# Optimization experiments

Measured on AMD Instinct MI355X. Metric: run time of the kernel, lower is better.

Reference implementation:

```python
import jax, jax.numpy as jnp
import numpy as np

B, T, D, H, L, O = 512, 512, 128, 256, 2, 1


def setup_inputs() -> dict:
    key = jax.random.key(0)
    ks = jax.random.split(key, 10)
    s = lambda fan_in: 1.0 / np.sqrt(fan_in)
    return {
        "x": jax.random.normal(ks[0], (B, T, D), jnp.float32),
        "h0": jax.random.normal(ks[1], (L, B, H), jnp.float32),
        "c0": jax.random.normal(ks[2], (L, B, H), jnp.float32),
        "wi_0": jax.random.normal(ks[3], (D, 4 * H), jnp.float32) * s(D),
        "hi_0": jax.random.normal(ks[4], (H, 4 * H), jnp.float32) * s(H),
        "bias_0": jnp.zeros((4 * H,), jnp.float32),
        "wi_1": jax.random.normal(ks[5], (H, 4 * H), jnp.float32) * s(H),
        "hi_1": jax.random.normal(ks[6], (H, 4 * H), jnp.float32) * s(H),
        "bias_1": jnp.zeros((4 * H,), jnp.float32),
        "fc_w": jax.random.normal(ks[7], (H, O), jnp.float32) * s(H),
        "fc_b": jnp.zeros((O,), jnp.float32),
    }


def _lstm_cell(x_t, h, c, wi, hi, b):
    # x_t: [B, Din], h/c: [B, H]
    gates = x_t @ wi + h @ hi + b  # [B, 4H]
    i_t = jax.nn.sigmoid(gates[:, :H])
    f_t = jax.nn.sigmoid(gates[:, H:2 * H])
    g_t = jnp.tanh(gates[:, 2 * H:3 * H])
    o_t = jax.nn.sigmoid(gates[:, 3 * H:])
    c_new = f_t * c + i_t * g_t
    h_new = o_t * jnp.tanh(c_new)
    return h_new, c_new


def reference(x, h0, c0, wi_0, hi_0, bias_0, wi_1, hi_1, bias_1, fc_w, fc_b):
    xs = jnp.transpose(x, (1, 0, 2))  # [T, B, D]
    layers = ((wi_0, hi_0, bias_0), (wi_1, hi_1, bias_1))

    def step(carry, x_t):
        hs, cs = carry  # each [L, B, H]
        new_h, new_c = [], []
        inp = x_t
        for i, (wi, hi, b) in enumerate(layers):
            h, c = _lstm_cell(inp, hs[i], cs[i], wi, hi, b)
            new_h.append(h)
            new_c.append(c)
            inp = h
        return (jnp.stack(new_h), jnp.stack(new_c)), None

    (hs, _), _ = jax.lax.scan(step, (h0, c0), xs)
    return hs[-1] @ fc_w + fc_b  # [B, O]
```

## Files before the change

kernel.cpp:

```cpp
#include <hip/hip_runtime.h>


#define G4 1024

typedef __bf16 bf16x8 __attribute__((ext_vector_type(8)));
typedef float f32x4 __attribute__((ext_vector_type(4)));
typedef unsigned short u16x8 __attribute__((ext_vector_type(8)));

#define MFMA(a, b, c) __builtin_amdgcn_mfma_f32_16x16x32_bf16(a, b, c, 0, 0, 0)
#define GIDX(r, c) ((c) ^ ((((r) >> 2) & 1) << 4))

__device__ __forceinline__ unsigned short f2bf(float f) {
  unsigned u = __builtin_bit_cast(unsigned, f);
  u += 0x7fffu + ((u >> 16) & 1u);
  return (unsigned short)(u >> 16);
}
__device__ __forceinline__ float bf2f(unsigned v) {
  v <<= 16;
  return __builtin_bit_cast(float, v);
}
__device__ __forceinline__ float sigm(float x) { return 1.f / (1.f + __expf(-x)); }
__device__ __forceinline__ float tanh_(float x) {
  float e = __expf(-2.f * fabsf(x));
  float t = (1.f - e) / (1.f + e);
  return (x < 0.f) ? -t : t;
}

template <int IMM>
__device__ __forceinline__ unsigned g_load_i(const unsigned* p) {
  unsigned r;
  asm volatile("global_load_dword %0, %1, off offset:%c2 sc0 sc1"
               : "=v"(r) : "v"(p), "i"(IMM) : "memory");
  return r;
}
__device__ __forceinline__ void g_store1(unsigned* p, unsigned v) {
  asm volatile("global_store_dword %0, %1, off sc0 sc1" ::"v"(p), "v"(v) : "memory");
}
__device__ __forceinline__ unsigned long long g_load2(const unsigned* p) {
  unsigned long long r;
  asm volatile("global_load_dwordx2 %0, %1, off sc0 sc1"
               : "=v"(r) : "v"(p) : "memory");
  return r;
}
__device__ __forceinline__ void g_store2(unsigned* p, unsigned long long v) {
  asm volatile("global_store_dwordx2 %0, %1, off sc0 sc1" ::"v"(p), "v"(v) : "memory");
}
#define VDRAIN()                                      \
  do {                                                \
    asm volatile("s_waitcnt vmcnt(0)" ::: "memory");  \
    __builtin_amdgcn_sched_barrier(0);                \
  } while (0)

#define LDH16(A, P)                                             \
  A[0] = g_load_i<0>(P);     A[1] = g_load_i<256>(P);           \
  A[2] = g_load_i<512>(P);   A[3] = g_load_i<768>(P);           \
  A[4] = g_load_i<1024>(P);  A[5] = g_load_i<1280>(P);          \
  A[6] = g_load_i<1536>(P);  A[7] = g_load_i<1792>(P);          \
  A[8] = g_load_i<2048>(P);  A[9] = g_load_i<2304>(P);          \
  A[10] = g_load_i<2560>(P); A[11] = g_load_i<2816>(P);         \
  A[12] = g_load_i<3072>(P); A[13] = g_load_i<3328>(P);         \
  A[14] = g_load_i<3584>(P); A[15] = g_load_i<3840>(P);

#define LDE16(A, P)                                             \
  A[0] = g_load_i<0>(P);    A[1] = g_load_i<32>(P);             \
  A[2] = g_load_i<64>(P);   A[3] = g_load_i<96>(P);             \
  A[4] = g_load_i<128>(P);  A[5] = g_load_i<160>(P);            \
  A[6] = g_load_i<192>(P);  A[7] = g_load_i<224>(P);            \
  A[8] = g_load_i<256>(P);  A[9] = g_load_i<288>(P);            \
  A[10] = g_load_i<320>(P); A[11] = g_load_i<352>(P);           \
  A[12] = g_load_i<384>(P); A[13] = g_load_i<416>(P);           \
  A[14] = g_load_i<448>(P); A[15] = g_load_i<480>(P);

extern "C" __global__ void __launch_bounds__(256, 1)
lstm_persist(const float* __restrict__ x, const float* __restrict__ h0in,
             const float* __restrict__ c0in, const float* __restrict__ wi0,
             const float* __restrict__ hi0, const float* __restrict__ b0,
             const float* __restrict__ wi1, const float* __restrict__ hi1,
             const float* __restrict__ b1, const float* __restrict__ fcw,
             const float* __restrict__ fcb, float* __restrict__ out,
             unsigned* ws_u32) {
  const int bid = blockIdx.x;
  const int grp = bid >> 4, n = bid & 15;
  const int row0 = grp * 32;
  const int hc0 = n * 16;
  const int tid = threadIdx.x;
  const int w = tid >> 6;
  const int lane = tid & 63;
  const int lc = lane & 15;
  const int kl = (lane >> 4) * 8;
  const int arow = lane & 15;
  const int ac = tid & 15, ar = tid >> 4;
  const int srow = 8 * w;

  unsigned* h0b = ws_u32;
  unsigned* h1b = ws_u32 + 131072;
  unsigned* flgP = ws_u32 + 262144;
  unsigned* fpw = flgP + grp * 128 + (n * 4 + w) * 2;

  __shared__ unsigned short x_lds[32][136];
  __shared__ unsigned short h0_lds[32][264];
  __shared__ unsigned short h1_lds[32][264];
  __shared__ float gates0[32][72];
  __shared__ float gates1[32][72];

  bf16x8 bw0[12];
  bf16x8 bw1[16];
  const int gcol = w * 256 + hc0 + lc;
  {
#pragma unroll
    for (int ks = 0; ks < 4; ++ks) {
      u16x8 v;
#pragma unroll
      for (int j = 0; j < 8; ++j) v[j] = f2bf(wi0[(ks * 32 + kl + j) * G4 + gcol]);
      bw0[ks] = __builtin_bit_cast(bf16x8, v);
    }
#pragma unroll
    for (int ks = 0; ks < 8; ++ks) {
      u16x8 v;
#pragma unroll
      for (int j = 0; j < 8; ++j) v[j] = f2bf(hi0[(ks * 32 + kl + j) * G4 + gcol]);
      bw0[4 + ks] = __builtin_bit_cast(bf16x8, v);
    }
#pragma unroll
    for (int ks = 0; ks < 8; ++ks) {
      u16x8 v;
#pragma unroll
      for (int j = 0; j < 8; ++j) v[j] = f2bf(wi1[(ks * 32 + kl + j) * G4 + gcol]);
      bw1[ks] = __builtin_bit_cast(bf16x8, v);
    }
#pragma unroll
    for (int ks = 0; ks < 8; ++ks) {
      u16x8 v;
#pragma unroll
      for (int j = 0; j < 8; ++j) v[j] = f2bf(hi1[(ks * 32 + kl + j) * G4 + gcol]);
      bw1[8 + ks] = __builtin_bit_cast(bf16x8, v);
    }
  }

  float bb0[4], bb1[4];
#pragma unroll
  for (int q = 0; q < 4; ++q) {
    bb0[q] = b0[q * 256 + hc0 + ac];
    bb1[q] = b1[q * 256 + hc0 + ac];
  }
  float c0r[2], c1r[2];
#pragma unroll
  for (int half = 0; half < 2; ++half) {
    int r = ar + half * 16, rg = row0 + r;
    c0r[half] = c0in[rg * 256 + hc0 + ac];
    c1r[half] = c0in[131072 + rg * 256 + hc0 + ac];
    unsigned short hb0s = f2bf(h0in[rg * 256 + hc0 + ac]);
    unsigned short hb1s = f2bf(h0in[131072 + rg * 256 + hc0 + ac]);
    unsigned o0 = (unsigned)__shfl_down((int)hb0s, 1) & 0xffffu;
    unsigned o1 = (unsigned)__shfl_down((int)hb1s, 1) & 0xffffu;
    if (!(ac & 1)) {
      unsigned ui = 65536u + (unsigned)(rg * 128) + (unsigned)((hc0 + ac) >> 1);
      g_store1(h0b + ui, (unsigned)hb0s | (o0 << 16));
      g_store1(h1b + ui, (unsigned)hb1s | (o1 << 16));
    }
  }
  VDRAIN();
  if (lane == 0) g_store2(fpw, 1ull | (2ull << 32));

  auto waitpair = [&](unsigned need0, unsigned need1) {
    const unsigned* p = flgP + grp * 128 + lane * 2;
    int sp = 0;
    for (;;) {
      unsigned long long v = g_load2(p);
      VDRAIN();
      unsigned f0 = (unsigned)v, f1 = (unsigned)(v >> 32);
      if (__all((int)((f0 >= need0) && (f1 >= need1)))) break;
      if (++sp >= (1 << 17)) break;
    }
  };

  float2 fr[8];
#pragma unroll
  for (int rr = 0; rr < 8; ++rr)
    fr[rr] = *(const float2*)(x + ((size_t)(row0 + srow + rr) << 16) + 2 * lane);
  VDRAIN();
#pragma unroll
  for (int rr = 0; rr < 8; ++rr) {
    unsigned p = (unsigned)f2bf(fr[rr].x) | ((unsigned)f2bf(fr[rr].y) << 16);
    ((unsigned*)&x_lds[srow + rr][0])[lane] = p;
  }
#pragma unroll
  for (int rr = 0; rr < 8; ++rr)
    fr[rr] = *(const float2*)(x + ((size_t)(row0 + srow + rr) << 16) + 128 + 2 * lane);
  __syncthreads();

  f32x4 p10{0.f, 0.f, 0.f, 0.f}, p11{0.f, 0.f, 0.f, 0.f};

  for (int i = 0; i < 514; ++i) {
    f32x4 a00{0.f, 0.f, 0.f, 0.f}, a01{0.f, 0.f, 0.f, 0.f};
    if (i < 512) {
#pragma unroll
      for (int ks = 0; ks < 4; ++ks) {
        bf16x8 a0 = *(const bf16x8*)&x_lds[arow][ks * 32 + kl];
        bf16x8 a1 = *(const bf16x8*)&x_lds[16 + arow][ks * 32 + kl];
        a00 = MFMA(a0, bw0[ks], a00);
        a01 = MFMA(a1, bw0[ks], a01);
      }
    }

    waitpair((unsigned)(i <= 512 ? i + 1 : 513), (unsigned)i);

    unsigned ta[16], tb[16];
    if (i <= 512) {
      const unsigned* hp0 = h0b + ((i + 1) & 1) * 65536 + (row0 + srow) * 128 + lane;
      LDH16(ta, hp0);
    }
    if (i >= 2) {
      const unsigned* hp1 = h1b + ((i + 1) & 1) * 65536 + (row0 + srow) * 128 + lane;
      LDH16(tb, hp1);
    }
    VDRAIN();
    if (i <= 512) {
#pragma unroll
      for (int rr = 0; rr < 8; ++rr) {
        unsigned* dst = (unsigned*)&h0_lds[srow + rr][0];
        dst[lane] = ta[2 * rr];
        dst[64 + lane] = ta[2 * rr + 1];
      }
    }
    if (i >= 2) {
#pragma unroll
      for (int rr = 0; rr < 8; ++rr) {
        unsigned* dst = (unsigned*)&h1_lds[srow + rr][0];
        dst[lane] = tb[2 * rr];
        dst[64 + lane] = tb[2 * rr + 1];
      }
    }
    __syncthreads();

    if (i <= 510) {
#pragma unroll
      for (int rr = 0; rr < 8; ++rr) {
        unsigned p = (unsigned)f2bf(fr[rr].x) | ((unsigned)f2bf(fr[rr].y) << 16);
        ((unsigned*)&x_lds[srow + rr][0])[lane] = p;
      }
    }
    if (i <= 509) {
#pragma unroll
      for (int rr = 0; rr < 8; ++rr)
        fr[rr] = *(const float2*)(x + ((size_t)(row0 + srow + rr) << 16) +
                                  (size_t)(i + 2) * 128 + 2 * lane);
    }
    f32x4 a10 = p10, a11 = p11;
    if (i < 512) {
#pragma unroll
      for (int ks = 0; ks < 8; ++ks) {
        bf16x8 a0 = *(const bf16x8*)&h0_lds[arow][ks * 32 + kl];
        bf16x8 a1 = *(const bf16x8*)&h0_lds[16 + arow][ks * 32 + kl];
        a00 = MFMA(a0, bw0[4 + ks], a00);
        a01 = MFMA(a1, bw0[4 + ks], a01);
      }
    }
    if (i >= 2) {
#pragma unroll
      for (int ks = 0; ks < 8; ++ks) {
        bf16x8 a0 = *(const bf16x8*)&h1_lds[arow][ks * 32 + kl];
        bf16x8 a1 = *(const bf16x8*)&h1_lds[16 + arow][ks * 32 + kl];
        a10 = MFMA(a0, bw1[8 + ks], a10);
        a11 = MFMA(a1, bw1[8 + ks], a11);
      }
    }
    if (i >= 1 && i <= 512) {
      p10 = f32x4{0.f, 0.f, 0.f, 0.f};
      p11 = f32x4{0.f, 0.f, 0.f, 0.f};
#pragma unroll
      for (int ks = 0; ks < 8; ++ks) {
        bf16x8 a0 = *(const bf16x8*)&h0_lds[arow][ks * 32 + kl];
        bf16x8 a1 = *(const bf16x8*)&h0_lds[16 + arow][ks * 32 + kl];
        p10 = MFMA(a0, bw1[ks], p10);
        p11 = MFMA(a1, bw1[ks], p11);
      }
    }
    {
      int col = w * 16 + lc;
      int rbase = (lane >> 4) * 4;
      if (i < 512) {
#pragma unroll
        for (int j = 0; j < 4; ++j) {
          gates0[rbase + j][GIDX(rbase + j, col)] = a00[j];
          gates0[16 + rbase + j][GIDX(16 + rbase + j, col)] = a01[j];
        }
      }
      if (i >= 2) {
#pragma unroll
        for (int j = 0; j < 4; ++j) {
          gates1[rbase + j][GIDX(rbase + j, col)] = a10[j];
          gates1[16 + rbase + j][GIDX(16 + rbase + j, col)] = a11[j];
        }
      }
    }
    __syncthreads();

    if (i < 512) {
#pragma unroll
      for (int half = 0; half < 2; ++half) {
        int r = ar + half * 16;
        float gi = gates0[r][GIDX(r, ac)] + bb0[0];
        float gf = gates0[r][GIDX(r, 16 + ac)] + bb0[1];
        float gg = gates0[r][GIDX(r, 32 + ac)] + bb0[2];
        float go = gates0[r][GIDX(r, 48 + ac)] + bb0[3];
        float ii = sigm(gi), ff = sigm(gf), g2 = tanh_(gg), oo = sigm(go);
        float c = ff * c0r[half] + ii * g2;
        c0r[half] = c;
        float h = oo * tanh_(c);
        unsigned short hb = f2bf(h);
        unsigned other = (unsigned)__shfl_down((int)hb, 1) & 0xffffu;
        if (!(ac & 1))
          g_store1(h0b + (i & 1) * 65536 + (row0 + r) * 128 + ((hc0 + ac) >> 1),
                   (unsigned)hb | (other << 16));
      }
    }
    if (i >= 2) {
#pragma unroll
      for (int half = 0; half < 2; ++half) {
        int r = ar + half * 16;
        float gi = gates1[r][GIDX(r, ac)] + bb1[0];
        float gf = gates1[r][GIDX(r, 16 + ac)] + bb1[1];
        float gg = gates1[r][GIDX(r, 32 + ac)] + bb1[2];
        float go = gates1[r][GIDX(r, 48 + ac)] + bb1[3];
        float ii = sigm(gi), ff = sigm(gf), g2 = tanh_(gg), oo = sigm(go);
        float c = ff * c1r[half] + ii * g2;
        c1r[half] = c;
        float h = oo * tanh_(c);
        unsigned short hb = f2bf(h);
        unsigned other = (unsigned)__shfl_down((int)hb, 1) & 0xffffu;
        if (!(ac & 1))
          g_store1(h1b + (i & 1) * 65536 + (row0 + r) * 128 + ((hc0 + ac) >> 1),
                   (unsigned)hb | (other << 16));
      }
    }

    VDRAIN();
    if (lane == 0) {
      unsigned f0v = (i < 512) ? (unsigned)(i + 2) : 513u;
      unsigned f1v = (i >= 2) ? (unsigned)(i + 1) : 2u;
      g_store2(fpw, (unsigned long long)f0v | ((unsigned long long)f1v << 32));
    }
  }

  if (n == 0) {
    waitpair(513u, 514u);
    int r = tid >> 3, sg = tid & 7;
    const unsigned* hrow = h1b + 65536 + (row0 + r) * 128 + sg;
    unsigned hv[16];
    LDE16(hv, hrow);
    VDRAIN();
    float sum = 0.f;
#pragma unroll
    for (int q = 0; q < 16; ++q) {
      int k2 = (sg + q * 8) * 2;
      sum += bf2f(hv[q] & 0xffffu) * fcw[k2];
      sum += bf2f(hv[q] >> 16) * fcw[k2 + 1];
    }
    sum += __shfl_down(sum, 4, 8);
    sum += __shfl_down(sum, 2, 8);
    sum += __shfl_down(sum, 1, 8);
    if (sg == 0) out[row0 + r] = sum + fcb[0];
  }
}

extern "C" void kernel_launch(void* const* d_in, const int* in_sizes, int n_in,
                              void* d_out, int out_size, void* d_ws, size_t ws_size,
                              hipStream_t stream) {
  hipMemsetAsync((char*)d_ws + 1048576, 0, 8192, stream);
  lstm_persist<<<dim3(256), dim3(256), 0, stream>>>(
      (const float*)d_in[0], (const float*)d_in[1], (const float*)d_in[2],
      (const float*)d_in[3], (const float*)d_in[4], (const float*)d_in[5],
      (const float*)d_in[6], (const float*)d_in[7], (const float*)d_in[8],
      (const float*)d_in[9], (const float*)d_in[10], (float*)d_out,
      (unsigned*)d_ws);
}
```

Measured before the change: 2.791 ms.

## Replace per-step flag barrier with tagged hidden-state words polled directly

Drops the separate flag array and the flag store/poll handshake. Each bf16 hidden value is now stored in its own 32-bit word with a step tag in the upper half. Consumers spin on dwordx4 loads of the data until every tag matches the expected step. This removes a drain, a flag store and a flag round-trip per step, plus the memset launch. In exchange it doubles the hidden-state traffic, and correctness depends on the stale tags left in the workspace from earlier runs never matching the expected values.

After: 3.255 ms. 16.6% more time.

```diff
diff --git a/kernel.cpp b/kernel.cpp
--- a/kernel.cpp
+++ b/kernel.cpp
@@ -6,6 +6,7 @@
 typedef __bf16 bf16x8 __attribute__((ext_vector_type(8)));
 typedef float f32x4 __attribute__((ext_vector_type(4)));
 typedef unsigned short u16x8 __attribute__((ext_vector_type(8)));
+typedef unsigned u32x4v __attribute__((ext_vector_type(4)));
 
 #define MFMA(a, b, c) __builtin_amdgcn_mfma_f32_16x16x32_bf16(a, b, c, 0, 0, 0)
 #define GIDX(r, c) ((c) ^ ((((r) >> 2) & 1) << 4))
@@ -27,23 +28,14 @@
 }
 
 template <int IMM>
-__device__ __forceinline__ unsigned g_load_i(const unsigned* p) {
-  unsigned r;
-  asm volatile("global_load_dword %0, %1, off offset:%c2 sc0 sc1"
+__device__ __forceinline__ u32x4v g_load4(const unsigned* p) {
+  u32x4v r;
+  asm volatile("global_load_dwordx4 %0, %1, off offset:%c2 sc0 sc1"
                : "=v"(r) : "v"(p), "i"(IMM) : "memory");
   return r;
 }
 __device__ __forceinline__ void g_store1(unsigned* p, unsigned v) {
   asm volatile("global_store_dword %0, %1, off sc0 sc1" ::"v"(p), "v"(v) : "memory");
-}
-__device__ __forceinline__ unsigned long long g_load2(const unsigned* p) {
-  unsigned long long r;
-  asm volatile("global_load_dwordx2 %0, %1, off sc0 sc1"
-               : "=v"(r) : "v"(p) : "memory");
-  return r;
-}
-__device__ __forceinline__ void g_store2(unsigned* p, unsigned long long v) {
-  asm volatile("global_store_dwordx2 %0, %1, off sc0 sc1" ::"v"(p), "v"(v) : "memory");
 }
 #define VDRAIN()                                      \
   do {                                                \
@@ -51,25 +43,25 @@
     __builtin_amdgcn_sched_barrier(0);                \
   } while (0)
 
-#define LDH16(A, P)                                             \
-  A[0] = g_load_i<0>(P);     A[1] = g_load_i<256>(P);           \
-  A[2] = g_load_i<512>(P);   A[3] = g_load_i<768>(P);           \
-  A[4] = g_load_i<1024>(P);  A[5] = g_load_i<1280>(P);          \
-  A[6] = g_load_i<1536>(P);  A[7] = g_load_i<1792>(P);          \
-  A[8] = g_load_i<2048>(P);  A[9] = g_load_i<2304>(P);          \
-  A[10] = g_load_i<2560>(P); A[11] = g_load_i<2816>(P);         \
-  A[12] = g_load_i<3072>(P); A[13] = g_load_i<3328>(P);         \
-  A[14] = g_load_i<3584>(P); A[15] = g_load_i<3840>(P);
-
-#define LDE16(A, P)                                             \
-  A[0] = g_load_i<0>(P);    A[1] = g_load_i<32>(P);             \
-  A[2] = g_load_i<64>(P);   A[3] = g_load_i<96>(P);             \
-  A[4] = g_load_i<128>(P);  A[5] = g_load_i<160>(P);            \
-  A[6] = g_load_i<192>(P);  A[7] = g_load_i<224>(P);            \
-  A[8] = g_load_i<256>(P);  A[9] = g_load_i<288>(P);            \
-  A[10] = g_load_i<320>(P); A[11] = g_load_i<352>(P);           \
-  A[12] = g_load_i<384>(P); A[13] = g_load_i<416>(P);           \
-  A[14] = g_load_i<448>(P); A[15] = g_load_i<480>(P);
+__device__ __forceinline__ void issue8(const unsigned* p, u32x4v* A) {
+  A[0] = g_load4<0>(p);
+  A[1] = g_load4<1024>(p);
+  A[2] = g_load4<2048>(p);
+  A[3] = g_load4<3072>(p);
+  const unsigned* q = p + 1024;
+  A[4] = g_load4<0>(q);
+  A[5] = g_load4<1024>(q);
+  A[6] = g_load4<2048>(q);
+  A[7] = g_load4<3072>(q);
+}
+__device__ __forceinline__ bool tagsok(const u32x4v* A, unsigned t) {
+  bool ok = true;
+#pragma unroll
+  for (int r2 = 0; r2 < 8; ++r2)
+#pragma unroll
+    for (int j = 0; j < 4; ++j) ok = ok && ((A[r2][j] >> 16) == t);
+  return ok;
+}
 
 extern "C" __global__ void __launch_bounds__(256, 1)
 lstm_persist(const float* __restrict__ x, const float* __restrict__ h0in,
@@ -92,10 +84,8 @@
   const int ac = tid & 15, ar = tid >> 4;
   const int srow = 8 * w;
 
-  unsigned* h0b = ws_u32;
-  unsigned* h1b = ws_u32 + 131072;
-  unsigned* flgP = ws_u32 + 262144;
-  unsigned* fpw = flgP + grp * 128 + (n * 4 + w) * 2;
+  unsigned* h0t = ws_u32;
+  unsigned* h1t = ws_u32 + 262144;
 
   __shared__ unsigned short x_lds[32][136];
   __shared__ unsigned short h0_lds[32][264];
@@ -151,28 +141,9 @@
     c1r[half] = c0in[131072 + rg * 256 + hc0 + ac];
     unsigned short hb0s = f2bf(h0in[rg * 256 + hc0 + ac]);
     unsigned short hb1s = f2bf(h0in[131072 + rg * 256 + hc0 + ac]);
-    unsigned o0 = (unsigned)__shfl_down((int)hb0s, 1) & 0xffffu;
-    unsigned o1 = (unsigned)__shfl_down((int)hb1s, 1) & 0xffffu;
-    if (!(ac & 1)) {
-      unsigned ui = 65536u + (unsigned)(rg * 128) + (unsigned)((hc0 + ac) >> 1);
-      g_store1(h0b + ui, (unsigned)hb0s | (o0 << 16));
-      g_store1(h1b + ui, (unsigned)hb1s | (o1 << 16));
-    }
-  }
-  VDRAIN();
-  if (lane == 0) g_store2(fpw, 1ull | (2ull << 32));
-
-  auto waitpair = [&](unsigned need0, unsigned need1) {
-    const unsigned* p = flgP + grp * 128 + lane * 2;
-    int sp = 0;
-    for (;;) {
-      unsigned long long v = g_load2(p);
-      VDRAIN();
-      unsigned f0 = (unsigned)v, f1 = (unsigned)(v >> 32);
-      if (__all((int)((f0 >= need0) && (f1 >= need1)))) break;
-      if (++sp >= (1 << 17)) break;
-    }
-  };
+    g_store1(h0t + 131072 + rg * 256 + hc0 + ac, (3u << 16) | (unsigned)hb0s);
+    g_store1(h1t + 131072 + rg * 256 + hc0 + ac, (3u << 16) | (unsigned)hb1s);
+  }
 
   float2 fr[8];
 #pragma unroll
@@ -203,32 +174,42 @@
       }
     }
 
-    waitpair((unsigned)(i <= 512 ? i + 1 : 513), (unsigned)i);
-
-    unsigned ta[16], tb[16];
-    if (i <= 512) {
-      const unsigned* hp0 = h0b + ((i + 1) & 1) * 65536 + (row0 + srow) * 128 + lane;
-      LDH16(ta, hp0);
-    }
-    if (i >= 2) {
-      const unsigned* hp1 = h1b + ((i + 1) & 1) * 65536 + (row0 + srow) * 128 + lane;
-      LDH16(tb, hp1);
-    }
-    VDRAIN();
-    if (i <= 512) {
+    const bool need0 = (i <= 512), need1 = (i >= 2);
+    const unsigned t0 = (unsigned)(i + 3), t1 = (unsigned)(i + 1);
+    const unsigned* hp0 =
+        h0t + ((i + 1) & 1) * 131072 + (row0 + srow) * 256 + 4 * lane;
+    const unsigned* hp1 =
+        h1t + ((i + 1) & 1) * 131072 + (row0 + srow) * 256 + 4 * lane;
+    u32x4v ha[8], hb[8];
+    if (need0) issue8(hp0, ha);
+    if (need1) issue8(hp1, hb);
+    {
+      int sp = 0;
+      for (;;) {
+        VDRAIN();
+        bool k0 = !need0 || __all((int)tagsok(ha, t0));
+        bool k1 = !need1 || __all((int)tagsok(hb, t1));
+        if ((k0 && k1) || ++sp >= (1 << 17)) break;
+        if (!k0) issue8(hp0, ha);
+        if (!k1) issue8(hp1, hb);
+      }
+    }
+    if (need0) {
 #pragma unroll
       for (int rr = 0; rr < 8; ++rr) {
-        unsigned* dst = (unsigned*)&h0_lds[srow + rr][0];
-        dst[lane] = ta[2 * rr];
-        dst[64 + lane] = ta[2 * rr + 1];
-      }
-    }
-    if (i >= 2) {
+        unsigned lo = (ha[rr][0] & 0xffffu) | (ha[rr][1] << 16);
+        unsigned hi = (ha[rr][2] & 0xffffu) | (ha[rr][3] << 16);
+        *(unsigned long long*)&((unsigned*)&h0_lds[srow + rr][0])[2 * lane] =
+            (unsigned long long)lo | ((unsigned long long)hi << 32);
+      }
+    }
+    if (need1) {
 #pragma unroll
       for (int rr = 0; rr < 8; ++rr) {
-        unsigned* dst = (unsigned*)&h1_lds[srow + rr][0];
-        dst[lane] = tb[2 * rr];
-        dst[64 + lane] = tb[2 * rr + 1];
+        unsigned lo = (hb[rr][0] & 0xffffu) | (hb[rr][1] << 16);
+        unsigned hi = (hb[rr][2] & 0xffffu) | (hb[rr][3] << 16);
+        *(unsigned long long*)&((unsigned*)&h1_lds[srow + rr][0])[2 * lane] =
+            (unsigned long long)lo | ((unsigned long long)hi << 32);
       }
     }
     __syncthreads();
@@ -297,6 +278,7 @@
     __syncthreads();
 
     if (i < 512) {
+      const unsigned tg0 = ((unsigned)(i + 4)) << 16;
 #pragma unroll
       for (int half = 0; half < 2; ++half) {
         int r = ar + half * 16;
@@ -308,14 +290,12 @@
         float c = ff * c0r[half] + ii * g2;
         c0r[half] = c;
         float h = oo * tanh_(c);
-        unsigned short hb = f2bf(h);
-        unsigned other = (unsigned)__shfl_down((int)hb, 1) & 0xffffu;
-        if (!(ac & 1))
-          g_store1(h0b + (i & 1) * 65536 + (row0 + r) * 128 + ((hc0 + ac) >> 1),
-                   (unsigned)hb | (other << 16));
+        g_store1(h0t + (i & 1) * 131072 + (row0 + r) * 256 + hc0 + ac,
+                 tg0 | (unsigned)f2bf(h));
       }
     }
     if (i >= 2) {
+      const unsigned tg1 = ((unsigned)(i + 2)) << 16;
 #pragma unroll
       for (int half = 0; half < 2; ++half) {
         int r = ar + half * 16;
@@ -327,47 +307,56 @@
         float c = ff * c1r[half] + ii * g2;
         c1r[half] = c;
         float h = oo * tanh_(c);
-        unsigned short hb = f2bf(h);
-        unsigned other = (unsigned)__shfl_down((int)hb, 1) & 0xffffu;
-        if (!(ac & 1))
-          g_store1(h1b + (i & 1) * 65536 + (row0 + r) * 128 + ((hc0 + ac) >> 1),
-                   (unsigned)hb | (other << 16));
-      }
-    }
-
-    VDRAIN();
-    if (lane == 0) {
-      unsigned f0v = (i < 512) ? (unsigned)(i + 2) : 513u;
-      unsigned f1v = (i >= 2) ? (unsigned)(i + 1) : 2u;
-      g_store2(fpw, (unsigned long long)f0v | ((unsigned long long)f1v << 32));
+        g_store1(h1t + (i & 1) * 131072 + (row0 + r) * 256 + hc0 + ac,
+                 tg1 | (unsigned)f2bf(h));
+      }
     }
   }
 
   if (n == 0) {
-    waitpair(513u, 514u);
-    int r = tid >> 3, sg = tid & 7;
-    const unsigned* hrow = h1b + 65536 + (row0 + r) * 128 + sg;
-    unsigned hv[16];
-    LDE16(hv, hrow);
-    VDRAIN();
+    int r2 = tid >> 3, sg = tid & 7;
+    const unsigned* hrow = h1t + 131072 + (row0 + r2) * 256 + sg * 4;
+    u32x4v hv[8];
+    auto issueE = [&]() {
+      hv[0] = g_load4<0>(hrow);
+      hv[1] = g_load4<128>(hrow);
+      hv[2] = g_load4<256>(hrow);
+      hv[3] = g_load4<384>(hrow);
+      hv[4] = g_load4<512>(hrow);
+      hv[5] = g_load4<640>(hrow);
+      hv[6] = g_load4<768>(hrow);
+      hv[7] = g_load4<896>(hrow);
+    };
+    issueE();
+    int sp = 0;
+    for (;;) {
+      VDRAIN();
+      bool ok = true;
+#pragma unroll
+      for (int q = 0; q < 8; ++q)
+#pragma unroll
+        for (int j = 0; j < 4; ++j) ok = ok && ((hv[q][j] >> 16) == 515u);
+      if (__all((int)ok) || ++sp >= (1 << 17)) break;
+      issueE();
+    }
     float sum = 0.f;
 #pragma unroll
-    for (int q = 0; q < 16; ++q) {
-      int k2 = (sg + q * 8) * 2;
-      sum += bf2f(hv[q] & 0xffffu) * fcw[k2];
-      sum += bf2f(hv[q] >> 16) * fcw[k2 + 1];
-    }
+    for (int q = 0; q < 8; ++q)
+#pragma unroll
+      for (int j = 0; j < 4; ++j) {
+        int col = sg * 4 + q * 32 + j;
+        sum += bf2f(hv[q][j] & 0xffffu) * fcw[col];
+      }
     sum += __shfl_down(sum, 4, 8);
     sum += __shfl_down(sum, 2, 8);
     sum += __shfl_down(sum, 1, 8);
-    if (sg == 0) out[row0 + r] = sum + fcb[0];
+    if (sg == 0) out[row0 + r2] = sum + fcb[0];
   }
 }
 
 extern "C" void kernel_launch(void* const* d_in, const int* in_sizes, int n_in,
                               void* d_out, int out_size, void* d_ws, size_t ws_size,
                               hipStream_t stream) {
-  hipMemsetAsync((char*)d_ws + 1048576, 0, 8192, stream);
   lstm_persist<<<dim3(256), dim3(256), 0, stream>>>(
       (const float*)d_in[0], (const float*)d_in[1], (const float*)d_in[2],
       (const float*)d_in[3], (const float*)d_in[4], (const float*)d_in[5],
```
